# Kernel tuning notes

Hardware: AMD Instinct MI355X
Metric: run time of the kernel (lower is better)

Reference implementation:

```python
import jax, jax.numpy as jnp
import numpy as np

N = 100_000      # nodes
E = 1_600_000    # edges
C_IN = 3         # pos dim
C = 128          # inter_dim == oup_dim
EPS = 1e-5       # BatchNorm eps


def setup_inputs() -> dict:
    key = jax.random.key(0)
    ks = iter(jax.random.split(key, 64))
    inp = {}
    inp['pos'] = jax.random.normal(next(ks), (N, C_IN), dtype=jnp.float32)
    inp['edge_index'] = jax.random.randint(next(ks), (2, E), 0, N, dtype=jnp.int32)
    dims = [C_IN, C, C, C, C]
    for i in range(1, 5):
        cin, cout = dims[i - 1], dims[i]
        inp[f'wl{i}'] = jax.random.normal(next(ks), (cin, cout), jnp.float32) * 0.05
        inp[f'bl{i}'] = jnp.zeros((cout,), jnp.float32)
        inp[f'wr{i}'] = jax.random.normal(next(ks), (cin, cout), jnp.float32) * 0.05
        inp[f'g{i}'] = jax.random.uniform(next(ks), (cout,), jnp.float32, 0.5, 1.5)
        inp[f'be{i}'] = jax.random.normal(next(ks), (cout,), jnp.float32) * 0.1
        inp[f'm{i}'] = jax.random.normal(next(ks), (cout,), jnp.float32) * 0.1
        inp[f'v{i}'] = jax.random.uniform(next(ks), (cout,), jnp.float32, 0.5, 1.5)
    for j, (cin, cout) in enumerate([(C, C), (C, C), (C, C)], start=1):
        inp[f'wf{j}'] = jax.random.normal(next(ks), (cin, cout), jnp.float32) * 0.05
        inp[f'bf{j}'] = jnp.zeros((cout,), jnp.float32)
    return inp


def _sage(x, src, dst, wl, bl, wr):
    # PyG SAGEConv: lin_l(mean_{j->i} x_j) + lin_r(x_i)
    msg_sum = jax.ops.segment_sum(x[src], dst, num_segments=N)          # [N, Cin]
    deg = jax.ops.segment_sum(jnp.ones((src.shape[0], 1), x.dtype), dst, num_segments=N)
    agg = msg_sum / jnp.maximum(deg, 1.0)
    return agg @ wl + bl + x @ wr


def _bn(x, g, b, m, v):
    return g * (x - m) * jax.lax.rsqrt(v + EPS) + b


def reference(pos, edge_index,
              wl1, bl1, wr1, g1, be1, m1, v1,
              wl2, bl2, wr2, g2, be2, m2, v2,
              wl3, bl3, wr3, g3, be3, m3, v3,
              wl4, bl4, wr4, g4, be4, m4, v4,
              wf1, bf1, wf2, bf2, wf3, bf3):
    src, dst = edge_index[0], edge_index[1]
    layers = [(wl1, bl1, wr1, g1, be1, m1, v1),
              (wl2, bl2, wr2, g2, be2, m2, v2),
              (wl3, bl3, wr3, g3, be3, m3, v3),
              (wl4, bl4, wr4, g4, be4, m4, v4)]
    x = pos
    for (wl, bl, wr, g, b, m, v) in layers:
        x = jax.nn.relu(_bn(_sage(x, src, dst, wl, bl, wr), g, b, m, v))
        # dropout p=0.1 inactive at inference
    x = x @ wf1 + bf1
    x = jax.nn.relu(x) @ wf2 + bf2
    x = x @ wf3 + bf3
    return x  # cls=False: raw output, no log_softmax
```

## Files before the change

kernel.cpp:

```cpp
#include <hip/hip_runtime.h>

#define NN 100000
#define EE 1600000
#define CC 128
#define NP 100032
#define NBK 782
#define BCAP 2304

typedef _Float16 f16;
typedef __attribute__((ext_vector_type(2))) f16 f16x2;
typedef __attribute__((ext_vector_type(4))) f16 f16x4;
typedef __attribute__((ext_vector_type(8))) f16 f16x8;
typedef __attribute__((ext_vector_type(4))) float f32x4;

#define MFMA16(a, b, c) __builtin_amdgcn_mfma_f32_16x16x32_f16(a, b, c, 0, 0, 0)


__global__ __launch_bounds__(1024) void k_part(const int* __restrict__ src,
                                               const int* __restrict__ dst,
                                               int* __restrict__ bcur,
                                               unsigned* __restrict__ bedge) {
  __shared__ int hist[NBK];
  __shared__ int base[NBK];
  const int t = threadIdx.x;
  for (int i = t; i < NBK; i += 1024) hist[i] = 0;
  __syncthreads();
  const int4* src4 = (const int4*)src;
  const int4* dst4 = (const int4*)dst;
  int4 s[4], d[4];
  int rk[16];
  bool val[4];
#pragma unroll
  for (int w = 0; w < 4; w++) {
    int i4 = blockIdx.x * 4096 + w * 1024 + t;
    val[w] = (i4 < EE / 4);
    if (val[w]) {
      s[w] = src4[i4];
      d[w] = dst4[i4];
      rk[w * 4 + 0] = atomicAdd(&hist[d[w].x >> 7], 1);
      rk[w * 4 + 1] = atomicAdd(&hist[d[w].y >> 7], 1);
      rk[w * 4 + 2] = atomicAdd(&hist[d[w].z >> 7], 1);
      rk[w * 4 + 3] = atomicAdd(&hist[d[w].w >> 7], 1);
    }
  }
  __syncthreads();
  for (int i = t; i < NBK; i += 1024) {
    int c = hist[i];
    base[i] = c ? atomicAdd(&bcur[i], c) : 0;
  }
  __syncthreads();
#pragma unroll
  for (int w = 0; w < 4; w++) {
    if (val[w]) {
      int ss[4] = {s[w].x, s[w].y, s[w].z, s[w].w};
      int dd[4] = {d[w].x, d[w].y, d[w].z, d[w].w};
#pragma unroll
      for (int q = 0; q < 4; q++) {
        int b = dd[q] >> 7;
        int slot = base[b] + rk[w * 4 + q];
        if (slot < BCAP)
          bedge[(size_t)b * BCAP + slot] =
              (unsigned)ss[q] | ((unsigned)(dd[q] & 127) << 17);
      }
    }
  }
}

__global__ __launch_bounds__(1024) void k_bscan(const int* __restrict__ bcur,
                                                int* __restrict__ bbase,
                                                int* __restrict__ off) {
  __shared__ int sh[1024];
  int t = threadIdx.x;
  int v = (t < NBK) ? min(bcur[t], BCAP) : 0;
  sh[t] = v;
  __syncthreads();
  for (int d = 1; d < 1024; d <<= 1) {
    int a = (t >= d) ? sh[t - d] : 0;
    __syncthreads();
    sh[t] += a;
    __syncthreads();
  }
  if (t < NBK) bbase[t] = sh[t] - v;
  if (t == 1023) off[NN] = sh[1023];
}

__global__ __launch_bounds__(256) void k_bfill2(const int* __restrict__ bcur,
                                                const int* __restrict__ bbase,
                                                const unsigned* __restrict__ bedge,
                                                int* __restrict__ off,
                                                int* __restrict__ csr) {
  __shared__ int h[128];
  __shared__ int sc[128];
  __shared__ int curs[128];
  const int b = blockIdx.x;
  const int t = threadIdx.x;
  if (t < 128) h[t] = 0;
  __syncthreads();
  const int cnt = min(bcur[b], BCAP);
  const unsigned* be = bedge + (size_t)b * BCAP;
  for (int i = t; i < cnt; i += 256) atomicAdd(&h[(be[i] >> 17) & 127], 1);
  __syncthreads();
  int v = (t < 128) ? h[t] : 0;
  if (t < 128) sc[t] = v;
  __syncthreads();
  for (int d = 1; d < 128; d <<= 1) {
    int a = (t >= d && t < 128) ? sc[t - d] : 0;
    __syncthreads();
    if (t < 128) sc[t] += a;
    __syncthreads();
  }
  if (t < 128) {
    int o = bbase[b] + sc[t] - v;
    int n = b * 128 + t;
    if (n < NN) off[n] = o;
    curs[t] = o;
  }
  __syncthreads();
  for (int i = t; i < cnt; i += 256) {
    unsigned u = be[i];
    int node = (u >> 17) & 127;
    int p = atomicAdd(&curs[node], 1);
    csr[p] = (int)(u & 0x1FFFF);
  }
}

struct WPtrs { const float* w[9]; };
__global__ __launch_bounds__(256) void k_packw(WPtrs wp, f16* __restrict__ out) {
  int t = blockIdx.x * 256 + threadIdx.x;
  int mat = t >> 14;
  int idx = t & 16383;
  int j = idx & 7;
  int lane = (idx >> 3) & 63;
  int ks = (idx >> 9) & 3;
  int nt = idx >> 11;
  int c16 = lane & 15, quad = lane >> 4;
  int k = ks * 32 + quad * 8 + j;
  int n = nt * 16 + c16;
  out[(size_t)mat * 16384 + idx] = (f16)wp.w[mat][k * CC + n];
}

__global__ __launch_bounds__(256) void k_agg3(const int* __restrict__ off,
                                              const int* __restrict__ csr,
                                              const float* __restrict__ pos,
                                              float* __restrict__ agg3) {
  int n = blockIdx.x * 256 + threadIdx.x;
  if (n >= NN) return;
  int b = off[n], e = off[n + 1];
  float a0 = 0.f, a1 = 0.f, a2 = 0.f;
  int i = b;
  for (; i + 4 <= e; i += 4) {
    int s0 = csr[i], s1 = csr[i + 1], s2 = csr[i + 2], s3 = csr[i + 3];
    float p00 = pos[s0 * 3 + 0], p01 = pos[s0 * 3 + 1], p02 = pos[s0 * 3 + 2];
    float p10 = pos[s1 * 3 + 0], p11 = pos[s1 * 3 + 1], p12 = pos[s1 * 3 + 2];
    float p20 = pos[s2 * 3 + 0], p21 = pos[s2 * 3 + 1], p22 = pos[s2 * 3 + 2];
    float p30 = pos[s3 * 3 + 0], p31 = pos[s3 * 3 + 1], p32 = pos[s3 * 3 + 2];
    a0 += (p00 + p10) + (p20 + p30);
    a1 += (p01 + p11) + (p21 + p31);
    a2 += (p02 + p12) + (p22 + p32);
  }
  for (; i < e; i++) {
    int s = csr[i];
    a0 += pos[s * 3 + 0];
    a1 += pos[s * 3 + 1];
    a2 += pos[s * 3 + 2];
  }
  float rd = 1.0f / fmaxf((float)(e - b), 1.0f);
  agg3[n * 3 + 0] = a0 * rd;
  agg3[n * 3 + 1] = a1 * rd;
  agg3[n * 3 + 2] = a2 * rd;
}

__global__ __launch_bounds__(256) void k_node1(
    const float* __restrict__ agg3, const float* __restrict__ pos,
    const float* __restrict__ wl, const float* __restrict__ bl,
    const float* __restrict__ wr, const float* __restrict__ g,
    const float* __restrict__ be, const float* __restrict__ bm,
    const float* __restrict__ bv, f16* __restrict__ x) {
  const int c = threadIdx.x & 127;
  const int np = threadIdx.x >> 7;
  const float Wl0 = wl[c], Wl1 = wl[CC + c], Wl2 = wl[2 * CC + c];
  const float Wr0 = wr[c], Wr1 = wr[CC + c], Wr2 = wr[2 * CC + c];
  const float sc = g[c] * rsqrtf(bv[c] + 1e-5f);
  const float o0 = be[c] + (bl[c] - bm[c]) * sc;
  const size_t sb = ((size_t)(c >> 4) * NP) * 16 + (c & 15);
  const int nbase = blockIdx.x * 256;
  const int nend = min(nbase + 256, NN);
#pragma unroll 4
  for (int n = nbase + np; n < nend; n += 2) {
    float acc = agg3[n * 3 + 0] * Wl0 + agg3[n * 3 + 1] * Wl1 +
                agg3[n * 3 + 2] * Wl2 + pos[n * 3 + 0] * Wr0 +
                pos[n * 3 + 1] * Wr1 + pos[n * 3 + 2] * Wr2;
    x[sb + (size_t)n * 16] = (f16)fmaxf(acc * sc + o0, 0.0f);
  }
}

__global__ __launch_bounds__(256) void k_agg_quad(const int* __restrict__ off,
                                                  const int* __restrict__ csr,
                                                  const f16* __restrict__ x,
                                                  f16* __restrict__ agg) {
  const int slab = blockIdx.x & 7;
  const int n = (blockIdx.x >> 3) * 64 + (threadIdx.x >> 2);
  const int cl = threadIdx.x & 3;
  if (n >= NN) return;
  const int b = off[n], e = off[n + 1];
  const f16* xs = x + (size_t)slab * NP * 16;
  float a[16];
#pragma unroll
  for (int j = 0; j < 16; j++) a[j] = 0.f;
  if (e > b) {
    int idx = csr[min(b + cl, e - 1)];
    for (int i = b; i < e; i += 4) {
      int idxn = 0;
      if (i + 4 < e) idxn = csr[min(i + 4 + cl, e - 1)];
      const f16* p = xs + (size_t)idx * 16;
      f16x8 v0 = *(const f16x8*)(p);
      f16x8 v1 = *(const f16x8*)(p + 8);
      if (i + cl < e) {
#pragma unroll
        for (int j = 0; j < 8; j++) a[j] += (float)v0[j];
#pragma unroll
        for (int j = 0; j < 8; j++) a[8 + j] += (float)v1[j];
      }
      idx = idxn;
    }
  }
#pragma unroll
  for (int j = 0; j < 16; j++) {
    a[j] += __shfl_xor(a[j], 1);
    a[j] += __shfl_xor(a[j], 2);
  }
  const float rd = 1.0f / fmaxf((float)(e - b), 1.0f);
  f16x4 o;
#pragma unroll
  for (int j = 0; j < 4; j++) o[j] = (f16)(a[cl * 4 + j] * rd);
  *(f16x4*)(agg + ((size_t)slab * NP + n) * 16 + cl * 4) = o;
}

__global__ __launch_bounds__(256) void k_sage_mfma(
    const f16* __restrict__ xin, f16* __restrict__ xout,
    const f16* __restrict__ agg, const f16* __restrict__ wl,
    const f16* __restrict__ wr, const float* __restrict__ bl,
    const float* __restrict__ g, const float* __restrict__ be,
    const float* __restrict__ bm, const float* __restrict__ bv) {
  const int lane = threadIdx.x & 63;
  const int wave = threadIdx.x >> 6;
  const int c16 = lane & 15;
  const int quad = lane >> 4;
  const int n0 = blockIdx.x * 64 + wave * 16;
  const int rowX = n0 + c16;
  const int rowA = min(rowX, NN - 1);
  f32x4 acc[8];
#pragma unroll
  for (int t = 0; t < 8; t++) acc[t] = {0.f, 0.f, 0.f, 0.f};
#pragma unroll
  for (int ks = 0; ks < 4; ks++) {
    const int cb = ks * 32 + quad * 8;
    const size_t sb = ((size_t)(cb >> 4) * NP) * 16 + (cb & 8);
    f16x8 Ax = *(const f16x8*)(xin + sb + (size_t)rowX * 16);
    f16x8 Aa = *(const f16x8*)(agg + sb + (size_t)rowA * 16);
#pragma unroll
    for (int nt = 0; nt < 8; nt++) {
      const size_t wo = (size_t)((nt * 4 + ks) * 64 + lane) * 8;
      f16x8 Bl = *(const f16x8*)(wl + wo);
      f16x8 Br = *(const f16x8*)(wr + wo);
      acc[nt] = MFMA16(Aa, Bl, acc[nt]);
      acc[nt] = MFMA16(Ax, Br, acc[nt]);
    }
  }
#pragma unroll
  for (int nt = 0; nt < 8; nt++) {
    const int col = nt * 16 + c16;
    const float blc = bl[col];
    const float sc = g[col] * rsqrtf(bv[col] + 1e-5f);
    const float mm = bm[col];
    const float bb = be[col];
#pragma unroll
    for (int r = 0; r < 4; r++) {
      const int node = n0 + quad * 4 + r;
      if (node < NN) {
        float yv = fmaxf((acc[nt][r] + blc - mm) * sc + bb, 0.0f);
        xout[((size_t)nt * NP + node) * 16 + c16] = (f16)yv;
      }
    }
  }
}

__global__ __launch_bounds__(256) void k_dense_fused(
    const f16* __restrict__ x, const f16* __restrict__ w1,
    const f16* __restrict__ w2, const f16* __restrict__ w3,
    const float* __restrict__ b1, const float* __restrict__ b2,
    const float* __restrict__ b3, float* __restrict__ out) {
  const int lane = threadIdx.x & 63;
  const int wave = threadIdx.x >> 6;
  const int c16 = lane & 15;
  const int quad = lane >> 4;
  const int n0 = blockIdx.x * 64 + wave * 16;
  const int lrow = wave * 16;
  __shared__ f16 sh[64][136];

  f32x4 acc[8];
#pragma unroll
  for (int t = 0; t < 8; t++) acc[t] = {0.f, 0.f, 0.f, 0.f};
  const int rowX = n0 + c16;
#pragma unroll
  for (int ks = 0; ks < 4; ks++) {
    const int cb = ks * 32 + quad * 8;
    const size_t sb = ((size_t)(cb >> 4) * NP) * 16 + (cb & 8);
    f16x8 Ax = *(const f16x8*)(x + sb + (size_t)rowX * 16);
#pragma unroll
    for (int nt = 0; nt < 8; nt++) {
      f16x8 B = *(const f16x8*)(w1 + (size_t)((nt * 4 + ks) * 64 + lane) * 8);
      acc[nt] = MFMA16(Ax, B, acc[nt]);
    }
  }
#pragma unroll
  for (int nt = 0; nt < 8; nt++) {
    const int col = nt * 16 + c16;
    const float bc = b1[col];
#pragma unroll
    for (int r = 0; r < 4; r++)
      sh[lrow + quad * 4 + r][col] = (f16)fmaxf(acc[nt][r] + bc, 0.0f);
  }
#pragma unroll
  for (int t = 0; t < 8; t++) acc[t] = {0.f, 0.f, 0.f, 0.f};
#pragma unroll
  for (int ks = 0; ks < 4; ks++) {
    f16x8 Ax = *(const f16x8*)&sh[lrow + c16][ks * 32 + quad * 8];
#pragma unroll
    for (int nt = 0; nt < 8; nt++) {
      f16x8 B = *(const f16x8*)(w2 + (size_t)((nt * 4 + ks) * 64 + lane) * 8);
      acc[nt] = MFMA16(Ax, B, acc[nt]);
    }
  }
#pragma unroll
  for (int nt = 0; nt < 8; nt++) {
    const int col = nt * 16 + c16;
    const float bc = b2[col];
#pragma unroll
    for (int r = 0; r < 4; r++)
      sh[lrow + quad * 4 + r][col] = (f16)(acc[nt][r] + bc);
  }
#pragma unroll
  for (int t = 0; t < 8; t++) acc[t] = {0.f, 0.f, 0.f, 0.f};
#pragma unroll
  for (int ks = 0; ks < 4; ks++) {
    f16x8 Ax = *(const f16x8*)&sh[lrow + c16][ks * 32 + quad * 8];
#pragma unroll
    for (int nt = 0; nt < 8; nt++) {
      f16x8 B = *(const f16x8*)(w3 + (size_t)((nt * 4 + ks) * 64 + lane) * 8);
      acc[nt] = MFMA16(Ax, B, acc[nt]);
    }
  }
#pragma unroll
  for (int nt = 0; nt < 8; nt++) {
    const int col = nt * 16 + c16;
    const float bc = b3[col];
#pragma unroll
    for (int r = 0; r < 4; r++) {
      const int node = n0 + quad * 4 + r;
      if (node < NN) out[(size_t)node * CC + col] = acc[nt][r] + bc;
    }
  }
}

extern "C" void kernel_launch(void* const* d_in, const int* in_sizes, int n_in,
                              void* d_out, int out_size, void* d_ws,
                              size_t ws_size, hipStream_t stream) {
  const float* pos = (const float*)d_in[0];
  const int* ei = (const int*)d_in[1];
  const int* src = ei;
  const int* dst = ei + EE;
  auto P = [&](int i) { return (const float*)d_in[i]; };

  int* bcur = (int*)d_ws;
  int* bbase = bcur + NBK;
  int* off = bbase + NBK;
  unsigned* bedge = (unsigned*)(off + NN + 2);
  int* csr = (int*)(bedge + (size_t)NBK * BCAP);
  f16* wp16 = (f16*)(csr + EE);
  f16* xa = wp16 + 9 * 16384;
  f16* xb = xa + (size_t)NP * CC;

  f16* agg = (f16*)d_out;

  hipMemsetAsync(bcur, 0, NBK * sizeof(int), stream);

  k_part<<<(EE / 4 + 4095) / 4096, 1024, 0, stream>>>(src, dst, bcur, bedge);
  k_bscan<<<1, 1024, 0, stream>>>(bcur, bbase, off);
  k_bfill2<<<NBK, 256, 0, stream>>>(bcur, bbase, bedge, off, csr);

  WPtrs wp;
  const int wsrc[9] = {9, 11, 16, 18, 23, 25, 30, 32, 34};
  for (int i = 0; i < 9; i++) wp.w[i] = P(wsrc[i]);
  k_packw<<<(9 * 16384) / 256, 256, 0, stream>>>(wp, wp16);

  k_agg3<<<(NN + 255) / 256, 256, 0, stream>>>(off, csr, pos, (float*)d_out);
  k_node1<<<(NN + 255) / 256, 256, 0, stream>>>(
      (const float*)d_out, pos, P(2), P(3), P(4), P(5), P(6), P(7), P(8), xa);

  const int NB = NP / 64;
  const f16* xi = xa;
  f16* xo = xb;
  for (int l = 1; l < 4; l++) {
    int base = 2 + 7 * l;
    int mat = (l - 1) * 2;
    k_agg_quad<<<NB * 8, 256, 0, stream>>>(off, csr, xi, agg);
    k_sage_mfma<<<NB, 256, 0, stream>>>(xi, xo, agg,
                                        wp16 + (size_t)mat * 16384,
                                        wp16 + (size_t)(mat + 1) * 16384,
                                        P(base + 1), P(base + 3), P(base + 4),
                                        P(base + 5), P(base + 6));
    const f16* t = xi;
    xi = xo;
    xo = (f16*)t;
  }

  k_dense_fused<<<NB, 256, 0, stream>>>(xi, wp16 + (size_t)6 * 16384,
                                        wp16 + (size_t)7 * 16384,
                                        wp16 + (size_t)8 * 16384, P(31), P(33),
                                        P(35), (float*)d_out);
}
```

Measured before the change: 607.9 us.

## Sort nodes by degree for aggregation and software-pipeline neighbor gathers

Adds a counting sort of nodes by descending in-degree, built from a histogram, a scan and a scatter, and has the aggregation kernel walk nodes in that order. Nodes with similar degree then share a wavefront, which cuts divergence and load imbalance in the gather loop. The gather loop is also restructured to prefetch the next neighbor's feature vectors one iteration ahead and to read CSR indices with nontemporal loads. This costs three extra small kernels plus a memset, and makes the writes to agg scattered rather than contiguous per block.

```diff
diff --git a/kernel.cpp b/kernel.cpp
--- a/kernel.cpp
+++ b/kernel.cpp
@@ -6,6 +6,7 @@
 #define NP 100032
 #define NBK 782
 #define BCAP 2304
+#define DBINS 1024
 
 typedef _Float16 f16;
 typedef __attribute__((ext_vector_type(2))) f16 f16x2;
@@ -122,6 +123,39 @@
     int p = atomicAdd(&curs[node], 1);
     csr[p] = (int)(u & 0x1FFFF);
   }
+}
+
+__global__ __launch_bounds__(256) void k_dhist(const int* __restrict__ off,
+                                               int* __restrict__ dh) {
+  int n = blockIdx.x * 256 + threadIdx.x;
+  if (n >= NN) return;
+  int deg = off[n + 1] - off[n];
+  int key = DBINS - 1 - min(deg, DBINS - 1);
+  atomicAdd(&dh[key], 1);
+}
+__global__ __launch_bounds__(1024) void k_dscan(int* __restrict__ dh) {
+  __shared__ int sh[DBINS];
+  int t = threadIdx.x;
+  int v = dh[t];
+  sh[t] = v;
+  __syncthreads();
+  for (int d = 1; d < DBINS; d <<= 1) {
+    int a = (t >= d) ? sh[t - d] : 0;
+    __syncthreads();
+    sh[t] += a;
+    __syncthreads();
+  }
+  dh[t] = sh[t] - v;
+}
+__global__ __launch_bounds__(256) void k_dscatter(const int* __restrict__ off,
+                                                  int* __restrict__ dh,
+                                                  int* __restrict__ perm) {
+  int n = blockIdx.x * 256 + threadIdx.x;
+  if (n >= NN) return;
+  int deg = off[n + 1] - off[n];
+  int key = DBINS - 1 - min(deg, DBINS - 1);
+  int p = atomicAdd(&dh[key], 1);
+  perm[p] = n;
 }
 
 struct WPtrs { const float* w[9]; };
@@ -196,32 +230,39 @@
 
 __global__ __launch_bounds__(256) void k_agg_quad(const int* __restrict__ off,
                                                   const int* __restrict__ csr,
+                                                  const int* __restrict__ perm,
                                                   const f16* __restrict__ x,
                                                   f16* __restrict__ agg) {
   const int slab = blockIdx.x & 7;
-  const int n = (blockIdx.x >> 3) * 64 + (threadIdx.x >> 2);
+  const int ns = (blockIdx.x >> 3) * 64 + (threadIdx.x >> 2);
   const int cl = threadIdx.x & 3;
-  if (n >= NN) return;
+  if (ns >= NN) return;
+  const int n = perm[ns];
   const int b = off[n], e = off[n + 1];
   const f16* xs = x + (size_t)slab * NP * 16;
   float a[16];
 #pragma unroll
   for (int j = 0; j < 16; j++) a[j] = 0.f;
   if (e > b) {
-    int idx = csr[min(b + cl, e - 1)];
+    const int last = e - 1;
+    int idx = __builtin_nontemporal_load(csr + min(b + cl, last));
+    int idxn = __builtin_nontemporal_load(csr + min(b + 4 + cl, last));
+    const f16* p0 = xs + (size_t)idx * 16;
+    f16x8 va = *(const f16x8*)(p0);
+    f16x8 vb = *(const f16x8*)(p0 + 8);
     for (int i = b; i < e; i += 4) {
-      int idxn = 0;
-      if (i + 4 < e) idxn = csr[min(i + 4 + cl, e - 1)];
-      const f16* p = xs + (size_t)idx * 16;
-      f16x8 v0 = *(const f16x8*)(p);
-      f16x8 v1 = *(const f16x8*)(p + 8);
+      const f16* pn = xs + (size_t)idxn * 16;
+      f16x8 wa = *(const f16x8*)(pn);
+      f16x8 wb = *(const f16x8*)(pn + 8);
+      idxn = __builtin_nontemporal_load(csr + min(i + 8 + cl, last));
       if (i + cl < e) {
 #pragma unroll
-        for (int j = 0; j < 8; j++) a[j] += (float)v0[j];
-#pragma unroll
-        for (int j = 0; j < 8; j++) a[8 + j] += (float)v1[j];
+        for (int j = 0; j < 8; j++) a[j] += (float)va[j];
+#pragma unroll
+        for (int j = 0; j < 8; j++) a[8 + j] += (float)vb[j];
       }
-      idx = idxn;
+      va = wa;
+      vb = wb;
     }
   }
 #pragma unroll
@@ -381,6 +422,9 @@
   f16* xa = wp16 + 9 * 16384;
   f16* xb = xa + (size_t)NP * CC;
 
+  int* dh = (int*)bedge;
+  int* perm = dh + DBINS;
+
   f16* agg = (f16*)d_out;
 
   hipMemsetAsync(bcur, 0, NBK * sizeof(int), stream);
@@ -388,6 +432,11 @@
   k_part<<<(EE / 4 + 4095) / 4096, 1024, 0, stream>>>(src, dst, bcur, bedge);
   k_bscan<<<1, 1024, 0, stream>>>(bcur, bbase, off);
   k_bfill2<<<NBK, 256, 0, stream>>>(bcur, bbase, bedge, off, csr);
+
+  hipMemsetAsync(dh, 0, DBINS * sizeof(int), stream);
+  k_dhist<<<(NN + 255) / 256, 256, 0, stream>>>(off, dh);
+  k_dscan<<<1, DBINS, 0, stream>>>(dh);
+  k_dscatter<<<(NN + 255) / 256, 256, 0, stream>>>(off, dh, perm);
 
   WPtrs wp;
   const int wsrc[9] = {9, 11, 16, 18, 23, 25, 30, 32, 34};
@@ -404,7 +453,7 @@
   for (int l = 1; l < 4; l++) {
     int base = 2 + 7 * l;
     int mat = (l - 1) * 2;
-    k_agg_quad<<<NB * 8, 256, 0, stream>>>(off, csr, xi, agg);
+    k_agg_quad<<<NB * 8, 256, 0, stream>>>(off, csr, perm, xi, agg);
     k_sage_mfma<<<NB, 256, 0, stream>>>(xi, xo, agg,
                                         wp16 + (size_t)mat * 16384,
                                         wp16 + (size_t)(mat + 1) * 16384,
```

After: 1.593 ms. 2.62x slower.
